# Performance work log

Measured on AMD Instinct MI355X. Metric: run time of the kernel, lower is better.

Reference implementation:

```python
import jax, jax.numpy as jnp
import numpy as np

# Model dims (match init_kwargs)
D_MODEL = 512
N_LAYERS = 4
N_DIST = 32
N_CAT = 32
LATENT = N_DIST * N_CAT  # 1024
D_INNER = 2 * D_MODEL    # 1024 (mamba expand=2)
D_STATE = 16
DT_RANK = D_MODEL // 16  # 32
K = 4                    # depthwise conv kernel
BATCH, SEQ = 4, 1024


def setup_inputs() -> dict:
    key = jax.random.key(0)
    ks = jax.random.split(key, 12)
    f = lambda k, shape, s=0.02: (jax.random.normal(k, shape, jnp.float32) * s)
    inp = {
        "x": jax.random.normal(ks[0], (BATCH, SEQ, LATENT), jnp.float32),
        "lin1_w": f(ks[1], (LATENT, D_MODEL)),
        "lin1_b": jnp.zeros((D_MODEL,), jnp.float32),
        "norm_w": jnp.ones((N_LAYERS, D_MODEL), jnp.float32),
        "in_w": f(ks[2], (N_LAYERS, D_MODEL, 2 * D_INNER)),
        "conv_w": f(ks[3], (N_LAYERS, D_INNER, K), 0.1),
        "conv_b": jnp.zeros((N_LAYERS, D_INNER), jnp.float32),
        "xproj_w": f(ks[4], (N_LAYERS, D_INNER, DT_RANK + 2 * D_STATE)),
        "dt_w": f(ks[5], (N_LAYERS, DT_RANK, D_INNER)),
        "dt_b": f(ks[6], (N_LAYERS, D_INNER), 0.5),
        "A_log": jnp.log(jnp.broadcast_to(
            jnp.arange(1, D_STATE + 1, dtype=jnp.float32),
            (N_LAYERS, D_INNER, D_STATE))),
        "Dp": jnp.ones((N_LAYERS, D_INNER), jnp.float32),
        "out_w": f(ks[7], (N_LAYERS, D_INNER, D_MODEL)),
        "lin2_w": f(ks[8], (D_MODEL, LATENT)),
        "lin2_b": jnp.zeros((LATENT,), jnp.float32),
    }
    return inp


def _rmsnorm(x, w):
    return x * jax.lax.rsqrt(jnp.mean(x * x, axis=-1, keepdims=True) + 1e-5) * w


def _causal_dwconv(x, w, b):
    # x: (B,S,D), w: (D,K) -> depthwise causal conv1d, left-padded
    S = x.shape[1]
    xp = jnp.pad(x, ((0, 0), (K - 1, 0), (0, 0)))
    y = xp[:, 0:S, :] * w[:, 0]
    for k in range(1, K):
        y = y + xp[:, k:k + S, :] * w[:, k]
    return y + b


def _selective_scan(u, dt, Bm, Cm, A, Dvec):
    # u, dt: (B,S,D); Bm, Cm: (B,S,N); A: (D,N); Dvec: (D,)
    dA = jnp.exp(dt[..., None] * A)                               # (B,S,D,N)
    dBu = dt[..., None] * Bm[:, :, None, :] * u[..., None]        # (B,S,D,N)
    h0 = jnp.zeros((u.shape[0], u.shape[2], A.shape[1]), u.dtype)

    def step(h, inputs):
        dA_t, dBu_t, C_t = inputs
        h = dA_t * h + dBu_t                                       # (B,D,N)
        y = jnp.einsum('bdn,bn->bd', h, C_t)
        return h, y

    _, ys = jax.lax.scan(step, h0,
                         (dA.transpose(1, 0, 2, 3),
                          dBu.transpose(1, 0, 2, 3),
                          Cm.transpose(1, 0, 2)))
    return ys.transpose(1, 0, 2) + u * Dvec                       # (B,S,D)


def reference(x, lin1_w, lin1_b, norm_w, in_w, conv_w, conv_b, xproj_w,
              dt_w, dt_b, A_log, Dp, out_w, lin2_w, lin2_b):
    B, S, _ = x.shape
    h = x @ lin1_w + lin1_b                                       # (B,S,d_model)
    for l in range(N_LAYERS):
        resid = h
        hn = _rmsnorm(h, norm_w[l])
        xz = hn @ in_w[l]                                         # (B,S,2*d_inner)
        xp, z = jnp.split(xz, 2, axis=-1)
        xp = jax.nn.silu(_causal_dwconv(xp, conv_w[l], conv_b[l]))
        dbl = xp @ xproj_w[l]                                     # (B,S,dt_rank+2N)
        dt = jax.nn.softplus(dbl[..., :DT_RANK] @ dt_w[l] + dt_b[l])
        Bm = dbl[..., DT_RANK:DT_RANK + D_STATE]
        Cm = dbl[..., DT_RANK + D_STATE:]
        A = -jnp.exp(A_log[l])                                    # (d_inner, N)
        y = _selective_scan(xp, dt, Bm, Cm, A, Dp[l])
        y = y * jax.nn.silu(z)
        h = resid + y @ out_w[l]
    out = h @ lin2_w + lin2_b                                     # (B,S,latent)
    out = jax.nn.softmax(out.reshape(B, S, N_DIST, N_CAT), axis=-1)
    return out.reshape(B, S, N_DIST * N_CAT)
```

## Files before the change

kernel.cpp:

```cpp
#include <hip/hip_runtime.h>
#include <math.h>

#define D_MODEL 512
#define N_LAYERS 4
#define LATENT 1024
#define D_INNER 1024
#define D_STATE 16
#define DT_RANK 32
#define KCONV 4
#define BATCH 4
#define SEQ 1024
#define NTOK (BATCH * SEQ)
#define PCH 32
#define CLEN 32

typedef __attribute__((ext_vector_type(8))) short short8;
typedef __attribute__((ext_vector_type(4))) float floatx4;
typedef unsigned short ushort_t;

#define WC_VM4   0x0F74
#define WC_VM8   0x0F78
#define WC_VM0   0x0F70
#define WC_LGKM0 0xC07F

__device__ __forceinline__ ushort_t f2bf(float f) {
    union { float f; unsigned u; } v; v.f = f;
    unsigned r = v.u + 0x7FFFu + ((v.u >> 16) & 1u);
    return (ushort_t)(r >> 16);
}
__device__ __forceinline__ float bf2f(ushort_t u) {
    union { unsigned u; float f; } v; v.u = ((unsigned)u) << 16;
    return v.f;
}
__device__ __forceinline__ void gll16(const void* g, void* l) {
    __builtin_amdgcn_global_load_lds(
        (const __attribute__((address_space(1))) void*)g,
        (__attribute__((address_space(3))) void*)l, 16, 0, 0);
}

__global__ __launch_bounds__(512, 2) void gemm_bf16_t256(
    const ushort_t* __restrict__ A, int lda,
    const ushort_t* __restrict__ Bt, int ldb,
    ushort_t* __restrict__ Cb, int ldc,
    int M, int N, int K)
{
    __shared__ ushort_t As[2][16384];
    __shared__ ushort_t Bs[2][16384];

    const int gx = gridDim.x;
    const int nwg = gx * gridDim.y;
    const int orig = blockIdx.y * gx + blockIdx.x;
    const int qq = nwg >> 3, rr = nwg & 7;
    const int xcd = orig & 7, loc = orig >> 3;
    const int swz = (xcd < rr ? xcd * (qq + 1) : rr * (qq + 1) + (xcd - rr) * qq) + loc;
    const int m0 = (swz / gx) * 256;
    const int n0 = (swz % gx) * 256;

    const int tid = threadIdx.x;
    const int w = tid >> 6;
    const int lane = tid & 63;
    const int quad = lane >> 4;
    const int l16 = lane & 15;
    const int wm = (w & 1) * 128;
    const int wn = (w >> 1) * 64;

    const int srow = tid >> 3;
    const int schunk = ((tid & 7) ^ (srow & 7)) * 8;
    const ushort_t* ga = A + (size_t)(m0 + srow) * lda + schunk;
    const ushort_t* gb = Bt + (size_t)(n0 + srow) * ldb + schunk;
    const int lofs = tid * 8;

    const int swz0 = ((0 * 4 + quad) ^ (l16 & 7)) * 8;
    const int swz1 = ((1 * 4 + quad) ^ (l16 & 7)) * 8;

    floatx4 acc[8][4] = {};
    const int nt = K >> 6;

    #define STAGE(t, b)                                                         \
        do {                                                                    \
            const ushort_t* pa_ = ga + (t) * 64;                                \
            const ushort_t* pb_ = gb + (t) * 64;                                \
            _Pragma("unroll")                                                   \
            for (int q = 0; q < 4; q++) {                                       \
                gll16(pa_ + (size_t)(q * 64) * lda, &As[(b)][q * 4096 + lofs]); \
                gll16(pb_ + (size_t)(q * 64) * ldb, &Bs[(b)][q * 4096 + lofs]); \
            }                                                                   \
        } while (0)

    STAGE(0, 0);

    for (int kt = 0; kt < nt; kt++) {
        const int cur = kt & 1;
        if (kt + 1 < nt) {
            STAGE(kt + 1, 1 - cur);
            __builtin_amdgcn_s_waitcnt(WC_VM8);
        } else {
            __builtin_amdgcn_s_waitcnt(WC_VM0);
        }
        __builtin_amdgcn_s_barrier();

        {
            short8 af[8], bfr[4];
            #pragma unroll
            for (int i = 0; i < 8; i++)
                af[i] = *(const short8*)&As[cur][(wm + i * 16 + l16) * 64 + swz0];
            #pragma unroll
            for (int j = 0; j < 4; j++)
                bfr[j] = *(const short8*)&Bs[cur][(wn + j * 16 + l16) * 64 + swz0];
            __builtin_amdgcn_s_waitcnt(WC_LGKM0);
            #pragma unroll
            for (int i = 0; i < 8; i++)
                #pragma unroll
                for (int j = 0; j < 4; j++)
                    acc[i][j] = __builtin_amdgcn_mfma_f32_16x16x32_bf16(
                        af[i], bfr[j], acc[i][j], 0, 0, 0);
        }
        {
            short8 af[8], bfr[4];
            #pragma unroll
            for (int i = 0; i < 8; i++)
                af[i] = *(const short8*)&As[cur][(wm + i * 16 + l16) * 64 + swz1];
            #pragma unroll
            for (int j = 0; j < 4; j++)
                bfr[j] = *(const short8*)&Bs[cur][(wn + j * 16 + l16) * 64 + swz1];
            __builtin_amdgcn_s_waitcnt(WC_LGKM0);
            #pragma unroll
            for (int i = 0; i < 8; i++)
                #pragma unroll
                for (int j = 0; j < 4; j++)
                    acc[i][j] = __builtin_amdgcn_mfma_f32_16x16x32_bf16(
                        af[i], bfr[j], acc[i][j], 0, 0, 0);
        }
        __builtin_amdgcn_s_barrier();
    }
    #undef STAGE

    #pragma unroll
    for (int j = 0; j < 4; j++) {
        int n = n0 + wn + j * 16 + l16;
        #pragma unroll
        for (int i = 0; i < 8; i++) {
            int mrow = m0 + wm + i * 16 + quad * 4;
            #pragma unroll
            for (int rr2 = 0; rr2 < 4; rr2++)
                Cb[(size_t)(mrow + rr2) * ldc + n] = f2bf(acc[i][j][rr2]);
        }
    }
}

__global__ __launch_bounds__(256, 3) void gemm_bf16_tile(
    const ushort_t* __restrict__ A, int lda,
    const ushort_t* __restrict__ Bt, int ldb,
    float* __restrict__ C, ushort_t* __restrict__ Cb, int ldc,
    const float* __restrict__ bias,
    int M, int N, int K, int flags)
{
    __shared__ ushort_t As[3][4096];
    __shared__ ushort_t Bs[3][4096];

    const int gx = gridDim.x;
    const int nwg = gx * gridDim.y;
    const int orig = blockIdx.y * gx + blockIdx.x;
    const int qq = nwg >> 3, rr = nwg & 7;
    const int xcd = orig & 7, loc = orig >> 3;
    const int swz = (xcd < rr ? xcd * (qq + 1) : rr * (qq + 1) + (xcd - rr) * qq) + loc;
    const int m0 = (swz / gx) * 64;
    const int n0 = (swz % gx) * 64;

    const int tid = threadIdx.x;
    const int w = tid >> 6;
    const int lane = tid & 63;
    const int quad = lane >> 4;
    const int l16 = lane & 15;
    const int wm = (w & 1) * 32;
    const int wn = (w >> 1) * 32;

    const int srow = tid >> 3;
    const int schunk = ((tid & 7) ^ (srow & 7)) * 8;
    const ushort_t* ga = A + (size_t)(m0 + srow) * lda + schunk;
    const ushort_t* gb = Bt + (size_t)(n0 + srow) * ldb + schunk;
    const int lofs = tid * 8;

    const int swz0 = ((0 * 4 + quad) ^ (l16 & 7)) * 8;
    const int swz1 = ((1 * 4 + quad) ^ (l16 & 7)) * 8;

    floatx4 acc[2][2] = {};
    const int nt = K >> 6;

    #define STAGE(t, b)                                         \
        do {                                                    \
            const ushort_t* pa_ = ga + (t) * 64;                \
            const ushort_t* pb_ = gb + (t) * 64;                \
            gll16(pa_, &As[(b)][lofs]);                         \
            gll16(pa_ + (size_t)32 * lda, &As[(b)][2048 + lofs]); \
            gll16(pb_, &Bs[(b)][lofs]);                         \
            gll16(pb_ + (size_t)32 * ldb, &Bs[(b)][2048 + lofs]); \
        } while (0)

    STAGE(0, 0);
    if (nt > 1) STAGE(1, 1);

    int cur = 0;
    for (int kt = 0; kt < nt; kt++) {
        if (kt + 1 < nt) __builtin_amdgcn_s_waitcnt(WC_VM4);
        else             __builtin_amdgcn_s_waitcnt(WC_VM0);
        __builtin_amdgcn_s_barrier();
        __builtin_amdgcn_sched_barrier(0);

        if (kt + 2 < nt) {
            int nb = cur + 2; if (nb >= 3) nb -= 3;
            STAGE(kt + 2, nb);
        }

        short8 af[2][2], bfr[2][2];
        #pragma unroll
        for (int i = 0; i < 2; i++) {
            const int r = wm + i * 16 + l16;
            af[0][i] = *(const short8*)&As[cur][r * 64 + swz0];
            af[1][i] = *(const short8*)&As[cur][r * 64 + swz1];
        }
        #pragma unroll
        for (int j = 0; j < 2; j++) {
            const int r = wn + j * 16 + l16;
            bfr[0][j] = *(const short8*)&Bs[cur][r * 64 + swz0];
            bfr[1][j] = *(const short8*)&Bs[cur][r * 64 + swz1];
        }
        __builtin_amdgcn_s_waitcnt(WC_LGKM0);
        __builtin_amdgcn_sched_barrier(0);

        #pragma unroll
        for (int ks = 0; ks < 2; ks++)
            #pragma unroll
            for (int i = 0; i < 2; i++)
                #pragma unroll
                for (int j = 0; j < 2; j++)
                    acc[i][j] = __builtin_amdgcn_mfma_f32_16x16x32_bf16(
                        af[ks][i], bfr[ks][j], acc[i][j], 0, 0, 0);

        cur++; if (cur == 3) cur = 0;
    }
    #undef STAGE

    if (flags & 32) {
        #pragma unroll
        for (int i = 0; i < 2; i++) {
            #pragma unroll
            for (int rr2 = 0; rr2 < 4; rr2++) {
                float v0 = acc[i][0][rr2] + bias[n0 + wn + l16];
                float v1 = acc[i][1][rr2] + bias[n0 + wn + 16 + l16];
                float m = fmaxf(v0, v1);
                #pragma unroll
                for (int off = 1; off < 16; off <<= 1)
                    m = fmaxf(m, __shfl_xor(m, off));
                float e0 = __expf(v0 - m), e1 = __expf(v1 - m);
                float s = e0 + e1;
                #pragma unroll
                for (int off = 1; off < 16; off <<= 1)
                    s += __shfl_xor(s, off);
                float inv = 1.f / s;
                size_t row = (size_t)(m0 + wm + i * 16 + quad * 4 + rr2) * ldc;
                C[row + n0 + wn + l16] = e0 * inv;
                C[row + n0 + wn + 16 + l16] = e1 * inv;
            }
        }
        return;
    }
    #pragma unroll
    for (int j = 0; j < 2; j++) {
        int n = n0 + wn + j * 16 + l16;
        float bv = (flags & 1) ? bias[n] : 0.f;
        bool do_sp = (flags & 4) && (n < 1024);
        float spb = do_sp ? bias[n] : 0.f;
        #pragma unroll
        for (int i = 0; i < 2; i++) {
            int mrow = m0 + wm + i * 16 + quad * 4;
            #pragma unroll
            for (int rr2 = 0; rr2 < 4; rr2++) {
                size_t idx = (size_t)(mrow + rr2) * ldc + n;
                float v = acc[i][j][rr2] + bv;
                if (do_sp) {
                    v += spb;
                    v = (v > 20.f) ? v : log1pf(__expf(v));
                }
                if (flags & 8) {
                    Cb[idx] = f2bf(v);
                } else {
                    if (flags & 2) v += C[idx];
                    C[idx] = v;
                    if (flags & 16) Cb[idx] = f2bf(v);
                }
            }
        }
    }
}

__global__ __launch_bounds__(256, 3) void gemm_stepA(
    const ushort_t* __restrict__ A,
    const ushort_t* __restrict__ Bt,
    float* __restrict__ Cpart)
{
    __shared__ ushort_t As[3][4096];
    __shared__ ushort_t Bs[3][4096];

    const int kq = blockIdx.x;
    const int m0 = blockIdx.y * 64;
    const int k0 = kq * 256;

    const int tid = threadIdx.x;
    const int w = tid >> 6;
    const int lane = tid & 63;
    const int quad = lane >> 4;
    const int l16 = lane & 15;
    const int wm = (w & 1) * 32;
    const int wn = (w >> 1) * 32;

    const int srow = tid >> 3;
    const int schunk = ((tid & 7) ^ (srow & 7)) * 8;
    const ushort_t* ga = A + (size_t)(m0 + srow) * 1024 + k0 + schunk;
    const ushort_t* gb = Bt + (size_t)srow * 1024 + k0 + schunk;
    const int lofs = tid * 8;

    const int swz0 = ((0 * 4 + quad) ^ (l16 & 7)) * 8;
    const int swz1 = ((1 * 4 + quad) ^ (l16 & 7)) * 8;

    floatx4 acc[2][2] = {};
    const int nt = 4;

    #define STAGE(t, b)                                            \
        do {                                                       \
            const ushort_t* pa_ = ga + (t) * 64;                   \
            const ushort_t* pb_ = gb + (t) * 64;                   \
            gll16(pa_, &As[(b)][lofs]);                            \
            gll16(pa_ + (size_t)32 * 1024, &As[(b)][2048 + lofs]); \
            gll16(pb_, &Bs[(b)][lofs]);                            \
            gll16(pb_ + (size_t)32 * 1024, &Bs[(b)][2048 + lofs]); \
        } while (0)

    STAGE(0, 0);
    STAGE(1, 1);

    int cur = 0;
    for (int kt = 0; kt < nt; kt++) {
        if (kt + 1 < nt) __builtin_amdgcn_s_waitcnt(WC_VM4);
        else             __builtin_amdgcn_s_waitcnt(WC_VM0);
        __builtin_amdgcn_s_barrier();
        __builtin_amdgcn_sched_barrier(0);

        if (kt + 2 < nt) {
            int nb = cur + 2; if (nb >= 3) nb -= 3;
            STAGE(kt + 2, nb);
        }

        short8 af[2][2], bfr[2][2];
        #pragma unroll
        for (int i = 0; i < 2; i++) {
            const int r = wm + i * 16 + l16;
            af[0][i] = *(const short8*)&As[cur][r * 64 + swz0];
            af[1][i] = *(const short8*)&As[cur][r * 64 + swz1];
        }
        #pragma unroll
        for (int j = 0; j < 2; j++) {
            const int r = wn + j * 16 + l16;
            bfr[0][j] = *(const short8*)&Bs[cur][r * 64 + swz0];
            bfr[1][j] = *(const short8*)&Bs[cur][r * 64 + swz1];
        }
        __builtin_amdgcn_s_waitcnt(WC_LGKM0);
        __builtin_amdgcn_sched_barrier(0);

        #pragma unroll
        for (int ks = 0; ks < 2; ks++)
            #pragma unroll
            for (int i = 0; i < 2; i++)
                #pragma unroll
                for (int j = 0; j < 2; j++)
                    acc[i][j] = __builtin_amdgcn_mfma_f32_16x16x32_bf16(
                        af[ks][i], bfr[ks][j], acc[i][j], 0, 0, 0);

        cur++; if (cur == 3) cur = 0;
    }
    #undef STAGE

    float* Cp = Cpart + (size_t)kq * NTOK * 64;
    #pragma unroll
    for (int j = 0; j < 2; j++) {
        int n = wn + j * 16 + l16;
        #pragma unroll
        for (int i = 0; i < 2; i++) {
            int mrow = m0 + wm + i * 16 + quad * 4;
            #pragma unroll
            for (int rr2 = 0; rr2 < 4; rr2++)
                Cp[(size_t)(mrow + rr2) * 64 + n] = acc[i][j][rr2];
        }
    }
}

__global__ __launch_bounds__(256, 3) void gemm_stepB(
    const float* __restrict__ part,
    const ushort_t* __restrict__ Bt,
    float* __restrict__ dblr,
    float* __restrict__ dtb,
    const float* __restrict__ bias)
{
    __shared__ ushort_t As[4096];
    __shared__ ushort_t Bs[4096];

    const int gx = gridDim.x;
    const int nwg = gx * gridDim.y;
    const int orig = blockIdx.y * gx + blockIdx.x;
    const int qq = nwg >> 3, rr = nwg & 7;
    const int xcd = orig & 7, loc = orig >> 3;
    const int swz = (xcd < rr ? xcd * (qq + 1) : rr * (qq + 1) + (xcd - rr) * qq) + loc;
    const int m0 = (swz / gx) * 64;
    const int n0 = (swz % gx) * 64;
    const bool wdblr = ((swz % gx) == 0);

    const int tid = threadIdx.x;
    const int w = tid >> 6;
    const int lane = tid & 63;
    const int quad = lane >> 4;
    const int l16 = lane & 15;
    const int wm = (w & 1) * 32;
    const int wn = (w >> 1) * 32;

    const int srow = tid >> 3;
    const int schunk = ((tid & 7) ^ (srow & 7)) * 8;
    const int lofs = tid * 8;

    const ushort_t* gb = Bt + (size_t)(n0 + srow) * 64 + schunk;
    gll16(gb, &Bs[lofs]);
    gll16(gb + (size_t)32 * 64, &Bs[2048 + lofs]);

    const size_t st = (size_t)NTOK * 64;
    const float* pa0 = part + (size_t)(m0 + srow) * 64 + schunk;
    const float* pa1 = pa0 + (size_t)32 * 64;
    floatx4 a0l = *(const floatx4*)(pa0);
    floatx4 a0h = *(const floatx4*)(pa0 + 4);
    floatx4 a1l = *(const floatx4*)(pa1);
    floatx4 a1h = *(const floatx4*)(pa1 + 4);
    #pragma unroll
    for (int kq = 1; kq < 4; kq++) {
        a0l += *(const floatx4*)(pa0 + (size_t)kq * st);
        a0h += *(const floatx4*)(pa0 + (size_t)kq * st + 4);
        a1l += *(const floatx4*)(pa1 + (size_t)kq * st);
        a1h += *(const floatx4*)(pa1 + (size_t)kq * st + 4);
    }
    short8 u0, u1;
    #pragma unroll
    for (int q = 0; q < 4; q++) {
        u0[q] = (short)f2bf(a0l[q]); u0[4 + q] = (short)f2bf(a0h[q]);
        u1[q] = (short)f2bf(a1l[q]); u1[4 + q] = (short)f2bf(a1h[q]);
    }
    *(short8*)&As[lofs] = u0;
    *(short8*)&As[2048 + lofs] = u1;
    if (wdblr) {
        float* d0 = dblr + (size_t)(m0 + srow) * 64 + schunk;
        *(floatx4*)(d0) = a0l;       *(floatx4*)(d0 + 4) = a0h;
        *(floatx4*)(d0 + 32 * 64) = a1l; *(floatx4*)(d0 + 32 * 64 + 4) = a1h;
    }
    __syncthreads();

    const int swz0 = ((0 * 4 + quad) ^ (l16 & 7)) * 8;
    const int swz1 = ((1 * 4 + quad) ^ (l16 & 7)) * 8;

    floatx4 acc[2][2] = {};
    short8 af[2][2], bfr[2][2];
    #pragma unroll
    for (int i = 0; i < 2; i++) {
        const int r = wm + i * 16 + l16;
        af[0][i] = *(const short8*)&As[r * 64 + swz0];
        af[1][i] = *(const short8*)&As[r * 64 + swz1];
    }
    #pragma unroll
    for (int j = 0; j < 2; j++) {
        const int r = wn + j * 16 + l16;
        bfr[0][j] = *(const short8*)&Bs[r * 64 + swz0];
        bfr[1][j] = *(const short8*)&Bs[r * 64 + swz1];
    }
    #pragma unroll
    for (int ks = 0; ks < 2; ks++)
        #pragma unroll
        for (int i = 0; i < 2; i++)
            #pragma unroll
            for (int j = 0; j < 2; j++)
                acc[i][j] = __builtin_amdgcn_mfma_f32_16x16x32_bf16(
                    af[ks][i], bfr[ks][j], acc[i][j], 0, 0, 0);

    #pragma unroll
    for (int j = 0; j < 2; j++) {
        int n = n0 + wn + j * 16 + l16;
        float spb = bias[n];
        #pragma unroll
        for (int i = 0; i < 2; i++) {
            int mrow = m0 + wm + i * 16 + quad * 4;
            #pragma unroll
            for (int rr2 = 0; rr2 < 4; rr2++) {
                float v = acc[i][j][rr2] + spb;
                v = (v > 20.f) ? v : log1pf(__expf(v));
                dtb[(size_t)(mrow + rr2) * 1024 + n] = v;
            }
        }
    }
}

__global__ __launch_bounds__(256) void prep_all(
    const float* __restrict__ lin1_w, const float* __restrict__ in_w,
    const float* __restrict__ out_w, const float* __restrict__ xproj_w,
    const float* __restrict__ lin2_w, const float* __restrict__ dt_w,
    const float* __restrict__ x,
    ushort_t* __restrict__ lin1_wt, ushort_t* __restrict__ in_wt,
    ushort_t* __restrict__ out_wt, ushort_t* __restrict__ xw_t,
    ushort_t* __restrict__ lin2_wt, ushort_t* __restrict__ w2t,
    ushort_t* __restrict__ xb)
{
    const int bid = blockIdx.x;
    const int tid = threadIdx.x;

    if (bid >= 8448) {
        const int i = ((bid - 8448) * 256 + tid) * 8;
        floatx4 a = *(const floatx4*)&x[i];
        floatx4 b = *(const floatx4*)&x[i + 4];
        short8 o;
        o[0] = (short)f2bf(a[0]); o[1] = (short)f2bf(a[1]);
        o[2] = (short)f2bf(a[2]); o[3] = (short)f2bf(a[3]);
        o[4] = (short)f2bf(b[0]); o[5] = (short)f2bf(b[1]);
        o[6] = (short)f2bf(b[2]); o[7] = (short)f2bf(b[3]);
        *(short8*)&xb[i] = o;
        return;
    }
    if (bid >= 7424) {
        const int idx = (bid - 7424) * 256 + tid;
        const int k = idx & 63;
        const int n = (idx >> 6) & 1023;
        const int l = idx >> 16;
        ushort_t v = 0;
        if (k < 32)
            v = f2bf(dt_w[((size_t)l * DT_RANK + k) * D_INNER + n]);
        w2t[((size_t)l * 1024 + n) * 64 + k] = v;
        return;
    }

    const float* in; ushort_t* out; int K, N, t;
    if (bid < 512) {
        in = lin1_w; out = lin1_wt; K = 1024; N = 512; t = bid;
    } else if (bid < 4608) {
        int lb = bid - 512, l = lb >> 10; t = lb & 1023;
        in = in_w + (size_t)l * 512 * 2048; out = in_wt + (size_t)l * 2048 * 512;
        K = 512; N = 2048;
    } else if (bid < 6656) {
        int lb = bid - 4608, l = lb >> 9; t = lb & 511;
        in = out_w + (size_t)l * 1024 * 512; out = out_wt + (size_t)l * 512 * 1024;
        K = 1024; N = 512;
    } else if (bid < 6912) {
        int lb = bid - 6656, l = lb >> 6; t = lb & 63;
        in = xproj_w + (size_t)l * 1024 * 64; out = xw_t + (size_t)l * 64 * 1024;
        K = 1024; N = 64;
    } else {
        in = lin2_w; out = lin2_wt; K = 512; N = 1024; t = bid - 6912;
    }
    const int gxt = N >> 5;
    const int n0 = (t % gxt) * 32, k0 = (t / gxt) * 32;

    __shared__ float tile[32][33];
    const int tx = tid & 31, ty = tid >> 5;
    #pragma unroll
    for (int i = 0; i < 4; i++)
        tile[ty + i * 8][tx] = in[(size_t)(k0 + ty + i * 8) * N + n0 + tx];
    __syncthreads();
    #pragma unroll
    for (int i = 0; i < 4; i++)
        out[(size_t)(n0 + ty + i * 8) * K + k0 + tx] = f2bf(tile[tx][ty + i * 8]);
}

__global__ __launch_bounds__(256) void rmsnorm_kernel(
    const float* __restrict__ x, const float* __restrict__ w,
    ushort_t* __restrict__ y)
{
    const int row = blockIdx.x;
    const float* xr = x + (size_t)row * D_MODEL;
    ushort_t* yr = y + (size_t)row * D_MODEL;
    const int tid = threadIdx.x;

    float2 v = *(const float2*)&xr[tid * 2];
    float ss = v.x * v.x + v.y * v.y;
    #pragma unroll
    for (int off = 32; off > 0; off >>= 1) ss += __shfl_down(ss, off);

    __shared__ float wsum[4];
    __shared__ float scale_s;
    int wid = tid >> 6, lane = tid & 63;
    if (lane == 0) wsum[wid] = ss;
    __syncthreads();
    if (tid == 0) {
        float tot = wsum[0] + wsum[1] + wsum[2] + wsum[3];
        scale_s = 1.0f / sqrtf(tot / (float)D_MODEL + 1e-5f);
    }
    __syncthreads();
    float sc = scale_s;
    float2 wv = *(const float2*)&w[tid * 2];
    ushort2 o;
    o.x = f2bf(v.x * sc * wv.x);
    o.y = f2bf(v.y * sc * wv.y);
    *(ushort2*)&yr[tid * 2] = o;
}

__global__ __launch_bounds__(256) void conv_silu_kernel(
    const ushort_t* __restrict__ xz, const float* __restrict__ w,
    const float* __restrict__ bconv, ushort_t* __restrict__ outb)
{
    const int idx = blockIdx.x * 256 + threadIdx.x;
    const int d0 = (idx & 127) * 8;
    const int row = idx >> 7;
    const int t = row & (SEQ - 1);
    const ushort_t* base = xz + (size_t)row * 2048 + d0;

    short8 xv[4];
    #pragma unroll
    for (int k = 0; k < KCONV; k++) {
        if (t + k - (KCONV - 1) >= 0)
            xv[k] = *(const short8*)(base + (ptrdiff_t)(k - (KCONV - 1)) * 2048);
        else
            xv[k] = short8{0, 0, 0, 0, 0, 0, 0, 0};
    }

    short8 o;
    #pragma unroll
    for (int q = 0; q < 8; q++) {
        floatx4 wq = *(const floatx4*)&w[(size_t)(d0 + q) * KCONV];
        float s = 0.f;
        #pragma unroll
        for (int k = 0; k < KCONV; k++)
            s = fmaf(bf2f((ushort_t)xv[k][q]), wq[k], s);
        s += bconv[d0 + q];
        float r = s / (1.f + __expf(-s));
        o[q] = (short)f2bf(r);
    }
    *(short8*)&outb[(size_t)row * D_INNER + d0] = o;
}

__global__ __launch_bounds__(256) void scan_pass1(
    const float* __restrict__ dtb, const float* __restrict__ bc,
    const ushort_t* __restrict__ ub, const float* __restrict__ A_log,
    float* __restrict__ hfin, float* __restrict__ sumdt)
{
    const int tid = threadIdx.x;
    const int b = blockIdx.x >> 7;
    const int p = (blockIdx.x >> 2) & 31;
    const int d = ((blockIdx.x & 3) << 8) + tid;
    const int t0 = p * CLEN;

    float A[D_STATE];
    #pragma unroll
    for (int n = 0; n < D_STATE; n++) A[n] = -expf(A_log[d * D_STATE + n]);

    float h[D_STATE] = {};
    float sdt = 0.f;

    const float* dtp = dtb + ((size_t)b * SEQ + t0) * 1024 + d;
    const float* bp  = bc + ((size_t)b * SEQ + t0) * 64 + 32;
    const ushort_t* up = ub + ((size_t)b * SEQ + t0) * D_INNER + d;

    for (int t = 0; t < CLEN; t++) {
        float dtv = dtp[(size_t)t * 1024];
        float uv  = bf2f(up[(size_t)t * D_INNER]);
        float dtu = dtv * uv;
        sdt += dtv;
        #pragma unroll
        for (int n = 0; n < D_STATE; n++)
            h[n] = fmaf(__expf(dtv * A[n]), h[n], dtu * bp[t * 64 + n]);
    }

    size_t base = (size_t)(b * PCH + p) * D_STATE * D_INNER + d;
    #pragma unroll
    for (int n = 0; n < D_STATE; n++) hfin[base + (size_t)n * D_INNER] = h[n];
    sumdt[(size_t)(b * PCH + p) * D_INNER + d] = sdt;
}

__global__ __launch_bounds__(256) void scan_pass2(
    const float* __restrict__ A_log, const float* __restrict__ sumdt,
    float* __restrict__ hc)
{
    const int tid = threadIdx.x;
    const int b = blockIdx.x >> 6;
    const int n = (blockIdx.x >> 2) & 15;
    const int d = ((blockIdx.x & 3) << 8) + tid;

    const float Aval = -expf(A_log[d * D_STATE + n]);

    float fin[PCH], sd[PCH];
    #pragma unroll
    for (int p = 0; p < PCH; p++) {
        fin[p] = hc[((size_t)(b * PCH + p) * D_STATE + n) * D_INNER + d];
        sd[p]  = sumdt[(size_t)(b * PCH + p) * D_INNER + d];
    }
    float h = 0.f;
    #pragma unroll
    for (int p = 0; p < PCH; p++) {
        hc[((size_t)(b * PCH + p) * D_STATE + n) * D_INNER + d] = h;
        h = fmaf(__expf(Aval * sd[p]), h, fin[p]);
    }
}

__global__ __launch_bounds__(256) void scan_pass3(
    const float* __restrict__ dtb, const float* __restrict__ bc,
    const ushort_t* __restrict__ xz, const float* __restrict__ A_log,
    const float* __restrict__ Dp, const float* __restrict__ hstart,
    ushort_t* ub)
{
    const int tid = threadIdx.x;
    const int b = blockIdx.x >> 7;
    const int p = (blockIdx.x >> 2) & 31;
    const int d = ((blockIdx.x & 3) << 8) + tid;
    const int t0 = p * CLEN;

    float A[D_STATE];
    #pragma unroll
    for (int n = 0; n < D_STATE; n++) A[n] = -expf(A_log[d * D_STATE + n]);
    const float Dv = Dp[d];

    float h[D_STATE];
    size_t base = (size_t)(b * PCH + p) * D_STATE * D_INNER + d;
    #pragma unroll
    for (int n = 0; n < D_STATE; n++) h[n] = hstart[base + (size_t)n * D_INNER];

    const float* dtp = dtb + ((size_t)b * SEQ + t0) * 1024 + d;
    const float* bp  = bc + ((size_t)b * SEQ + t0) * 64 + 32;
    const ushort_t* zp = xz + ((size_t)b * SEQ + t0) * 2048 + 1024 + d;
    ushort_t* up = ub + ((size_t)b * SEQ + t0) * D_INNER + d;

    for (int t = 0; t < CLEN; t++) {
        float dtv = dtp[(size_t)t * 1024];
        float uv  = bf2f(up[(size_t)t * D_INNER]);
        float zv  = bf2f(zp[(size_t)t * 2048]);
        float dtu = dtv * uv;
        float y = 0.f;
        #pragma unroll
        for (int n = 0; n < D_STATE; n++) {
            h[n] = fmaf(__expf(dtv * A[n]), h[n], dtu * bp[t * 64 + n]);
            y = fmaf(h[n], bp[t * 64 + 16 + n], y);
        }
        float res = fmaf(uv, Dv, y);
        res *= zv / (1.f + __expf(-zv));
        up[(size_t)t * D_INNER] = f2bf(res);
    }
}

extern "C" void kernel_launch(void* const* d_in, const int* in_sizes, int n_in,
                              void* d_out, int out_size, void* d_ws, size_t ws_size,
                              hipStream_t stream)
{
    const float* x       = (const float*)d_in[0];
    const float* lin1_w  = (const float*)d_in[1];
    const float* lin1_b  = (const float*)d_in[2];
    const float* norm_w  = (const float*)d_in[3];
    const float* in_w    = (const float*)d_in[4];
    const float* conv_w  = (const float*)d_in[5];
    const float* conv_b  = (const float*)d_in[6];
    const float* xproj_w = (const float*)d_in[7];
    const float* dt_w    = (const float*)d_in[8];
    const float* dt_b    = (const float*)d_in[9];
    const float* A_log   = (const float*)d_in[10];
    const float* Dp      = (const float*)d_in[11];
    const float* out_w   = (const float*)d_in[12];
    const float* lin2_w  = (const float*)d_in[13];
    const float* lin2_b  = (const float*)d_in[14];
    float* outp = (float*)d_out;
    (void)ws_size; (void)in_sizes; (void)n_in; (void)out_size;

    float* ws = (float*)d_ws;
    const size_t F1M = 1u << 20;
    float* h     = ws;
    float* dtb   = h + 2 * F1M;
    float* dblr  = dtb + 4 * F1M;
    float* dpart = dblr + (size_t)NTOK * 64;
    float* sumdt = dpart + (size_t)4 * NTOK * 64;
    float* hfin  = sumdt + (size_t)BATCH * PCH * D_INNER;
    ushort_t* xzb     = (ushort_t*)(hfin + 2 * F1M);
    ushort_t* hn_bf   = xzb + 8 * F1M;
    ushort_t* xb      = hn_bf + 2 * F1M;
    ushort_t* dblr_bf = xb + 4 * F1M;
    ushort_t* lin1_wt = dblr_bf + (size_t)NTOK * 64;
    ushort_t* in_wt   = lin1_wt + (size_t)512 * 1024;
    ushort_t* out_wt  = in_wt + (size_t)4 * 2048 * 512;
    ushort_t* lin2_wt = out_wt + (size_t)4 * 512 * 1024;
    ushort_t* xw_t    = lin2_wt + (size_t)1024 * 512;
    ushort_t* w2t     = xw_t + (size_t)4 * 64 * 1024;

    dim3 blk(256);

    prep_all<<<dim3(10496), blk, 0, stream>>>(
        lin1_w, in_w, out_w, xproj_w, lin2_w, dt_w, x,
        lin1_wt, in_wt, out_wt, xw_t, lin2_wt, w2t, xb);

    gemm_bf16_tile<<<dim3(D_MODEL / 64, NTOK / 64), blk, 0, stream>>>(
        xb, LATENT, lin1_wt, LATENT, h, nullptr, D_MODEL, lin1_b,
        NTOK, D_MODEL, LATENT, 1);

    for (int l = 0; l < N_LAYERS; l++) {
        const float* nw = norm_w + (size_t)l * D_MODEL;
        const float* cw = conv_w + (size_t)l * D_INNER * KCONV;
        const float* cb = conv_b + (size_t)l * D_INNER;
        const float* db = dt_b + (size_t)l * D_INNER;
        const float* al = A_log + (size_t)l * D_INNER * D_STATE;
        const float* dp = Dp + (size_t)l * D_INNER;
        const ushort_t* iwt = in_wt + (size_t)l * 2048 * 512;
        const ushort_t* owt = out_wt + (size_t)l * 512 * 1024;
        const ushort_t* xwt = xw_t + (size_t)l * 64 * 1024;
        const ushort_t* w2  = w2t + (size_t)l * 1024 * 64;

        rmsnorm_kernel<<<dim3(NTOK), blk, 0, stream>>>(h, nw, hn_bf);

        gemm_bf16_t256<<<dim3(2048 / 256, NTOK / 256), dim3(512), 0, stream>>>(
            hn_bf, D_MODEL, iwt, D_MODEL, xzb, 2048, NTOK, 2048, D_MODEL);

        conv_silu_kernel<<<dim3((NTOK * D_INNER) / 2048), blk, 0, stream>>>(
            xzb, cw, cb, xb);

        gemm_stepA<<<dim3(4, NTOK / 64), blk, 0, stream>>>(xb, xwt, dpart);

        gemm_stepB<<<dim3(1024 / 64, NTOK / 64), blk, 0, stream>>>(
            dpart, w2, dblr, dtb, db);

        scan_pass1<<<dim3(BATCH * PCH * (D_INNER / 256)), blk, 0, stream>>>(
            dtb, dblr, xb, al, hfin, sumdt);
        scan_pass2<<<dim3(BATCH * D_STATE * (D_INNER / 256)), blk, 0, stream>>>(
            al, sumdt, hfin);
        scan_pass3<<<dim3(BATCH * PCH * (D_INNER / 256)), blk, 0, stream>>>(
            dtb, dblr, xzb, al, dp, hfin, xb);

        gemm_bf16_tile<<<dim3(D_MODEL / 64, NTOK / 64), blk, 0, stream>>>(
            xb, D_INNER, owt, D_INNER, h, hn_bf, D_MODEL, nullptr,
            NTOK, D_MODEL, D_INNER, (l == N_LAYERS - 1) ? 18 : 2);
    }

    gemm_bf16_tile<<<dim3(LATENT / 64, NTOK / 64), blk, 0, stream>>>(
        hn_bf, D_MODEL, lin2_wt, D_MODEL, outp, nullptr, LATENT, lin2_b,
        NTOK, LATENT, D_MODEL, 1 | 32);
}
```

Before: 637.1 us.

## Fuse causal depthwise conv and SiLU into the x-projection GEMM prologue

Removes the standalone conv+SiLU kernel. The x-projection split-K GEMM now computes the convolved, SiLU-activated activations directly into shared memory, writing them to global memory as a side output for the scan. The whole 256-wide K slice is staged at once (four LDS buffers, lower occupancy bound), which drops the software pipeline. This saves a launch and a round trip of the activation tensor, at the cost of register and LDS pressure and global loads that are no longer overlapped with MFMA.

```diff
diff --git a/kernel.cpp b/kernel.cpp
--- a/kernel.cpp
+++ b/kernel.cpp
@@ -294,79 +294,93 @@
     }
 }
 
-__global__ __launch_bounds__(256, 3) void gemm_stepA(
-    const ushort_t* __restrict__ A,
+__global__ __launch_bounds__(256, 2) void gemm_stepA_conv(
+    const ushort_t* __restrict__ xz,
+    const float* __restrict__ w,
+    const float* __restrict__ bconv,
     const ushort_t* __restrict__ Bt,
+    ushort_t* __restrict__ ub,
     float* __restrict__ Cpart)
 {
-    __shared__ ushort_t As[3][4096];
-    __shared__ ushort_t Bs[3][4096];
+    __shared__ ushort_t As[4][4096];
+    __shared__ ushort_t Bs[4][4096];
 
     const int kq = blockIdx.x;
     const int m0 = blockIdx.y * 64;
     const int k0 = kq * 256;
 
     const int tid = threadIdx.x;
-    const int w = tid >> 6;
+    const int wv = tid >> 6;
     const int lane = tid & 63;
     const int quad = lane >> 4;
     const int l16 = lane & 15;
-    const int wm = (w & 1) * 32;
-    const int wn = (w >> 1) * 32;
+    const int wm = (wv & 1) * 32;
+    const int wn = (wv >> 1) * 32;
 
     const int srow = tid >> 3;
     const int schunk = ((tid & 7) ^ (srow & 7)) * 8;
-    const ushort_t* ga = A + (size_t)(m0 + srow) * 1024 + k0 + schunk;
-    const ushort_t* gb = Bt + (size_t)srow * 1024 + k0 + schunk;
     const int lofs = tid * 8;
+
+    #pragma unroll
+    for (int s = 0; s < 4; s++) {
+        const ushort_t* gb = Bt + (size_t)srow * 1024 + k0 + s * 64 + schunk;
+        gll16(gb, &Bs[s][lofs]);
+        gll16(gb + (size_t)32 * 1024, &Bs[s][2048 + lofs]);
+    }
+
+    #pragma unroll
+    for (int s = 0; s < 4; s++) {
+        #pragma unroll
+        for (int half = 0; half < 2; half++) {
+            const int row = m0 + srow + half * 32;
+            const int t = row & (SEQ - 1);
+            const int d0 = k0 + s * 64 + schunk;
+            short8 xv[4];
+            #pragma unroll
+            for (int k = 0; k < KCONV; k++) {
+                if (t + k - (KCONV - 1) >= 0)
+                    xv[k] = *(const short8*)(xz +
+                        (size_t)(row + k - (KCONV - 1)) * 2048 + d0);
+                else
+                    xv[k] = short8{0, 0, 0, 0, 0, 0, 0, 0};
+            }
+            short8 o;
+            #pragma unroll
+            for (int q = 0; q < 8; q++) {
+                floatx4 wq = *(const floatx4*)&w[(size_t)(d0 + q) * KCONV];
+                float sa = 0.f;
+                #pragma unroll
+                for (int k = 0; k < KCONV; k++)
+                    sa = fmaf(bf2f((ushort_t)xv[k][q]), wq[k], sa);
+                sa += bconv[d0 + q];
+                float r = sa / (1.f + __expf(-sa));
+                o[q] = (short)f2bf(r);
+            }
+            *(short8*)&As[s][half * 2048 + lofs] = o;
+            *(short8*)&ub[(size_t)row * D_INNER + d0] = o;
+        }
+    }
+    __syncthreads();
 
     const int swz0 = ((0 * 4 + quad) ^ (l16 & 7)) * 8;
     const int swz1 = ((1 * 4 + quad) ^ (l16 & 7)) * 8;
 
     floatx4 acc[2][2] = {};
-    const int nt = 4;
-
-    #define STAGE(t, b)                                            \
-        do {                                                       \
-            const ushort_t* pa_ = ga + (t) * 64;                   \
-            const ushort_t* pb_ = gb + (t) * 64;                   \
-            gll16(pa_, &As[(b)][lofs]);                            \
-            gll16(pa_ + (size_t)32 * 1024, &As[(b)][2048 + lofs]); \
-            gll16(pb_, &Bs[(b)][lofs]);                            \
-            gll16(pb_ + (size_t)32 * 1024, &Bs[(b)][2048 + lofs]); \
-        } while (0)
-
-    STAGE(0, 0);
-    STAGE(1, 1);
-
-    int cur = 0;
-    for (int kt = 0; kt < nt; kt++) {
-        if (kt + 1 < nt) __builtin_amdgcn_s_waitcnt(WC_VM4);
-        else             __builtin_amdgcn_s_waitcnt(WC_VM0);
-        __builtin_amdgcn_s_barrier();
-        __builtin_amdgcn_sched_barrier(0);
-
-        if (kt + 2 < nt) {
-            int nb = cur + 2; if (nb >= 3) nb -= 3;
-            STAGE(kt + 2, nb);
-        }
-
+    #pragma unroll
+    for (int s = 0; s < 4; s++) {
         short8 af[2][2], bfr[2][2];
         #pragma unroll
         for (int i = 0; i < 2; i++) {
             const int r = wm + i * 16 + l16;
-            af[0][i] = *(const short8*)&As[cur][r * 64 + swz0];
-            af[1][i] = *(const short8*)&As[cur][r * 64 + swz1];
+            af[0][i] = *(const short8*)&As[s][r * 64 + swz0];
+            af[1][i] = *(const short8*)&As[s][r * 64 + swz1];
         }
         #pragma unroll
         for (int j = 0; j < 2; j++) {
             const int r = wn + j * 16 + l16;
-            bfr[0][j] = *(const short8*)&Bs[cur][r * 64 + swz0];
-            bfr[1][j] = *(const short8*)&Bs[cur][r * 64 + swz1];
-        }
-        __builtin_amdgcn_s_waitcnt(WC_LGKM0);
-        __builtin_amdgcn_sched_barrier(0);
-
+            bfr[0][j] = *(const short8*)&Bs[s][r * 64 + swz0];
+            bfr[1][j] = *(const short8*)&Bs[s][r * 64 + swz1];
+        }
         #pragma unroll
         for (int ks = 0; ks < 2; ks++)
             #pragma unroll
@@ -375,10 +389,7 @@
                 for (int j = 0; j < 2; j++)
                     acc[i][j] = __builtin_amdgcn_mfma_f32_16x16x32_bf16(
                         af[ks][i], bfr[ks][j], acc[i][j], 0, 0, 0);
-
-        cur++; if (cur == 3) cur = 0;
-    }
-    #undef STAGE
+    }
 
     float* Cp = Cpart + (size_t)kq * NTOK * 64;
     #pragma unroll
@@ -601,40 +612,6 @@
     o.x = f2bf(v.x * sc * wv.x);
     o.y = f2bf(v.y * sc * wv.y);
     *(ushort2*)&yr[tid * 2] = o;
-}
-
-__global__ __launch_bounds__(256) void conv_silu_kernel(
-    const ushort_t* __restrict__ xz, const float* __restrict__ w,
-    const float* __restrict__ bconv, ushort_t* __restrict__ outb)
-{
-    const int idx = blockIdx.x * 256 + threadIdx.x;
-    const int d0 = (idx & 127) * 8;
-    const int row = idx >> 7;
-    const int t = row & (SEQ - 1);
-    const ushort_t* base = xz + (size_t)row * 2048 + d0;
-
-    short8 xv[4];
-    #pragma unroll
-    for (int k = 0; k < KCONV; k++) {
-        if (t + k - (KCONV - 1) >= 0)
-            xv[k] = *(const short8*)(base + (ptrdiff_t)(k - (KCONV - 1)) * 2048);
-        else
-            xv[k] = short8{0, 0, 0, 0, 0, 0, 0, 0};
-    }
-
-    short8 o;
-    #pragma unroll
-    for (int q = 0; q < 8; q++) {
-        floatx4 wq = *(const floatx4*)&w[(size_t)(d0 + q) * KCONV];
-        float s = 0.f;
-        #pragma unroll
-        for (int k = 0; k < KCONV; k++)
-            s = fmaf(bf2f((ushort_t)xv[k][q]), wq[k], s);
-        s += bconv[d0 + q];
-        float r = s / (1.f + __expf(-s));
-        o[q] = (short)f2bf(r);
-    }
-    *(short8*)&outb[(size_t)row * D_INNER + d0] = o;
 }
 
 __global__ __launch_bounds__(256) void scan_pass1(
@@ -812,10 +789,8 @@
         gemm_bf16_t256<<<dim3(2048 / 256, NTOK / 256), dim3(512), 0, stream>>>(
             hn_bf, D_MODEL, iwt, D_MODEL, xzb, 2048, NTOK, 2048, D_MODEL);
 
-        conv_silu_kernel<<<dim3((NTOK * D_INNER) / 2048), blk, 0, stream>>>(
-            xzb, cw, cb, xb);
-
-        gemm_stepA<<<dim3(4, NTOK / 64), blk, 0, stream>>>(xb, xwt, dpart);
+        gemm_stepA_conv<<<dim3(4, NTOK / 64), blk, 0, stream>>>(
+            xzb, cw, cb, xwt, xb, dpart);
 
         gemm_stepB<<<dim3(1024 / 64, NTOK / 64), blk, 0, stream>>>(
             dpart, w2, dblr, dtb, db);
```

Measured after the change: 628.1 us. About the same (-1.4%).
